# Kernel optimization log

Hardware: AMD Instinct MI355X
Metric: run time of the kernel (lower is better)

Reference implementation:

```python
import jax, jax.numpy as jnp
import numpy as np

B, S, D_IN, D_OUT, DEPTH = 4, 2048, 2048, 2048, 11
N_NODES = 2 ** (DEPTH + 1) - 1  # 4095


def setup_inputs() -> dict:
    key = jax.random.key(0)
    k1, k2, k3 = jax.random.split(key, 3)
    x = jax.random.normal(k1, (B, S, D_IN), dtype=jnp.float32)
    # scale weights like Linear init (~1/sqrt(fan_in)) to keep logits sane
    w_in = jax.random.normal(k2, (N_NODES, D_IN), dtype=jnp.float32) * (1.0 / np.sqrt(D_IN))
    w_out = jax.random.normal(k3, (D_OUT, N_NODES), dtype=jnp.float32) * (1.0 / np.sqrt(N_NODES))
    return {"x": x, "w_in": w_in, "w_out": w_out}


def reference(x, w_in, w_out):
    # x: [B,S,D_in]; w_in: [n_nodes, D_in]; w_out: [D_out, n_nodes]
    b, s, _ = x.shape
    cur = jnp.zeros((b, s), dtype=jnp.int32)
    nodes, logits = [], []
    for _ in range(DEPTH + 1):  # fixed, small depth loop (12 iters)
        nodes.append(cur)
        coeffs = w_in[cur]                       # [B,S,D_in] data-dependent gather
        score = jnp.einsum('bsd,bsd->bs', x, coeffs)  # per-token dot product
        logits.append(score)
        cur = cur * 2 + (score >= 0).astype(jnp.int32) + 1
    all_nodes = jnp.stack(nodes, axis=-1)        # [B,S,depth+1]
    all_logits = jnp.stack(logits, axis=-1)      # [B,S,depth+1]
    sel = w_out.T[all_nodes]                     # [B,S,depth+1,D_out]
    mlp1 = jax.nn.gelu(all_logits, approximate=False)  # torch nn.GELU default = exact erf
    return jnp.einsum('bsl,bslw->bsw', mlp1, sel)      # [B,S,D_out]
```

## Files before the change

### kernel.cpp

```cpp
#include <hip/hip_runtime.h>


#define D_IN    2048
#define D_OUT   2048
#define DEPTHP1 12
#define N_NODES 4095
#define N_TOK   8192
#define N_LEAF  2048

typedef float f4 __attribute__((ext_vector_type(4)));

__global__ __launch_bounds__(256, 4) void fusedA3(
    const float* __restrict__ x,
    const float* __restrict__ w_in,
    const float* __restrict__ w_out,
    float* __restrict__ w_out_t,
    float* __restrict__ s_all,
    int* __restrict__ leaf,
    int* __restrict__ hist) {
    if (blockIdx.x & 1) {
        __shared__ float tile[64][65];
        const int tb = blockIdx.x >> 1;
        const int n0 = (tb & 63) * 64;
        const int j0 = (tb >> 6) * 64;
        const int tx = threadIdx.x & 63;
        const int ty = threadIdx.x >> 6;
        const int n = n0 + tx;
#pragma unroll
        for (int k = 0; k < 16; k++) {
            const int r = ty * 16 + k;
            if (n < N_NODES) tile[r][tx] = w_out[(size_t)(j0 + r) * N_NODES + n];
        }
        __syncthreads();
#pragma unroll
        for (int k = 0; k < 16; k++) {
            const int r = ty * 16 + k;
            const int nn = n0 + r;
            if (nn < N_NODES) w_out_t[(size_t)nn * D_OUT + (j0 + tx)] = tile[tx][r];
        }
        return;
    }

    const int wave  = threadIdx.x >> 6;
    const int lane  = threadIdx.x & 63;
    const int token = (blockIdx.x >> 1) * 4 + wave;

    const float4* xrow = (const float4*)(x + (size_t)token * D_IN);
    float4 xf[8];
#pragma unroll
    for (int c = 0; c < 8; c++) xf[c] = xrow[lane + 64 * c];

    const unsigned voffA = (unsigned)lane * 16u;
    const unsigned voffB = voffA + 4096u;

    int cur = 0;
    float sc[DEPTHP1];
#pragma unroll
    for (int l = 0; l < DEPTHP1; l++) {
        const float* wbase = w_in + (size_t)cur * D_IN;
        f4 w0, w1, w2, w3, w4, w5, w6, w7;
        asm volatile("global_load_dwordx4 %0, %1, %2"             : "=v"(w0) : "v"(voffA), "s"(wbase));
        asm volatile("global_load_dwordx4 %0, %1, %2 offset:1024" : "=v"(w1) : "v"(voffA), "s"(wbase));
        asm volatile("global_load_dwordx4 %0, %1, %2 offset:2048" : "=v"(w2) : "v"(voffA), "s"(wbase));
        asm volatile("global_load_dwordx4 %0, %1, %2 offset:3072" : "=v"(w3) : "v"(voffA), "s"(wbase));
        asm volatile("global_load_dwordx4 %0, %1, %2"             : "=v"(w4) : "v"(voffB), "s"(wbase));
        asm volatile("global_load_dwordx4 %0, %1, %2 offset:1024" : "=v"(w5) : "v"(voffB), "s"(wbase));
        asm volatile("global_load_dwordx4 %0, %1, %2 offset:2048" : "=v"(w6) : "v"(voffB), "s"(wbase));
        asm volatile("global_load_dwordx4 %0, %1, %2 offset:3072" : "=v"(w7) : "v"(voffB), "s"(wbase));
        asm volatile("s_waitcnt vmcnt(0)"
                     : "+v"(w0), "+v"(w1), "+v"(w2), "+v"(w3),
                       "+v"(w4), "+v"(w5), "+v"(w6), "+v"(w7)
                     :: "memory");

        float p0 = 0.f, p1 = 0.f, p2 = 0.f, p3 = 0.f;
        p0 += w0[0]*xf[0].x + w0[1]*xf[0].y + w0[2]*xf[0].z + w0[3]*xf[0].w;
        p0 += w1[0]*xf[1].x + w1[1]*xf[1].y + w1[2]*xf[1].z + w1[3]*xf[1].w;
        p1 += w2[0]*xf[2].x + w2[1]*xf[2].y + w2[2]*xf[2].z + w2[3]*xf[2].w;
        p1 += w3[0]*xf[3].x + w3[1]*xf[3].y + w3[2]*xf[3].z + w3[3]*xf[3].w;
        p2 += w4[0]*xf[4].x + w4[1]*xf[4].y + w4[2]*xf[4].z + w4[3]*xf[4].w;
        p2 += w5[0]*xf[5].x + w5[1]*xf[5].y + w5[2]*xf[5].z + w5[3]*xf[5].w;
        p3 += w6[0]*xf[6].x + w6[1]*xf[6].y + w6[2]*xf[6].z + w6[3]*xf[6].w;
        p3 += w7[0]*xf[7].x + w7[1]*xf[7].y + w7[2]*xf[7].z + w7[3]*xf[7].w;
        float part = (p0 + p1) + (p2 + p3);
#pragma unroll
        for (int off = 32; off >= 1; off >>= 1)
            part += __shfl_xor(part, off, 64);
        const float score = part;
        cur = __builtin_amdgcn_readfirstlane(
                  2 * cur + 1 + (score >= 0.f ? 1 : 0));
        sc[l] = score;
    }
    if (lane == 0) {
        f4* sp = (f4*)(s_all + (size_t)token * DEPTHP1);
        f4 a = {sc[0], sc[1], sc[2],  sc[3]};
        f4 b = {sc[4], sc[5], sc[6],  sc[7]};
        f4 c = {sc[8], sc[9], sc[10], sc[11]};
        sp[0] = a; sp[1] = b; sp[2] = c;
        const int leafid = ((cur - 1) >> 1) - (N_LEAF - 1);
        leaf[token] = leafid;
        atomicAdd(&hist[leafid], 1);
    }
}

__global__ __launch_bounds__(256) void init_counts(int* __restrict__ p) {
    const int i = blockIdx.x * 256 + threadIdx.x;
    if (i < 2 * N_LEAF) p[i] = 0;
}

__global__ __launch_bounds__(256) void scan2048(
    const int* __restrict__ hist, int* __restrict__ offsets ) {
    __shared__ int vals[N_LEAF];
    __shared__ int partial[256];
    const int t = threadIdx.x;
    int sum = 0;
#pragma unroll
    for (int k = 0; k < 8; k++) {
        const int v = hist[t * 8 + k];
        vals[t * 8 + k] = v;
        sum += v;
    }
    partial[t] = sum;
    __syncthreads();
    for (int off = 1; off < 256; off <<= 1) {
        const int v  = partial[t];
        const int vo = (t >= off) ? partial[t - off] : 0;
        __syncthreads();
        partial[t] = v + vo;
        __syncthreads();
    }
    int base = (t > 0) ? partial[t - 1] : 0;
#pragma unroll
    for (int k = 0; k < 8; k++) {
        offsets[t * 8 + k] = base;
        base += vals[t * 8 + k];
    }
    if (t == 255) offsets[N_LEAF] = base;
}

__global__ __launch_bounds__(256) void scatter_tokens3(
    const int* __restrict__ leaf, const int* __restrict__ offsets,
    int* __restrict__ cnt, const float* __restrict__ s_all,
    int* __restrict__ order, float* __restrict__ g_sorted,
    int* __restrict__ lf_sorted) {
    const int t = blockIdx.x * 256 + threadIdx.x;
    if (t < N_TOK) {
        const int lf = leaf[t];
        const int pos = offsets[lf] + atomicAdd(&cnt[lf], 1);
        order[pos] = t;
        lf_sorted[pos] = lf;
#pragma unroll
        for (int l = 0; l < DEPTHP1; l++) {
            const float s = s_all[(size_t)t * DEPTHP1 + l];
            const float g = 0.5f * s * (1.0f + erff(s * 0.70710678118654752f));
            g_sorted[(size_t)pos * DEPTHP1 + l] = g;
        }
    }
}

__global__ __launch_bounds__(256, 2) void phaseB4(
    const float* __restrict__ w_out_t,
    const float* __restrict__ g_sorted,
    const int* __restrict__ lf_sorted,
    const int* __restrict__ order,
    const int* __restrict__ offsets,
    float* __restrict__ out) {
    const int grp = ((blockIdx.x & 7) << 6) | (blockIdx.x >> 3);
    const int lf0 = grp * 4;
    const int start = offsets[lf0];
    const int end   = offsets[lf0 + 4];
    if (start == end) return;
    const int t = threadIdx.x;

    __shared__ float wlds[16 * 1024];
    __shared__ float gslot[2][8][16];
    __shared__ int   ordl[2][8];

    int node[16];
    const int base1 = lf0 + N_LEAF;
#pragma unroll
    for (int l = 0; l <= 9; l++) node[l] = (base1 >> (11 - l)) - 1;
    node[10] = (base1 >> 1) - 1;
    node[11] = (base1 >> 1);
    node[12] = base1 - 1;
    node[13] = base1;
    node[14] = base1 + 1;
    node[15] = base1 + 2;

    for (int half = 0; half < 2; half++) {
        __syncthreads();
#pragma unroll
        for (int k = 0; k < 16; k++)
            ((f4*)wlds)[k * 256 + t] =
                ((const f4*)(w_out_t + (size_t)node[k] * D_OUT + half * 1024))[t];
        __syncthreads();

        int buf = 0;
        for (int cs = start; cs < end; cs += 8, buf ^= 1) {
            if (t < 8) {
                const int pos = cs + t;
#pragma unroll
                for (int s = 0; s < 16; s++) gslot[buf][t][s] = 0.f;
                if (pos < end) {
                    const int lf = lf_sorted[pos];
#pragma unroll
                    for (int l = 0; l <= 9; l++)
                        gslot[buf][t][l] = g_sorted[(size_t)pos * DEPTHP1 + l];
                    gslot[buf][t][10 + ((lf >> 1) & 1)] =
                        g_sorted[(size_t)pos * DEPTHP1 + 10];
                    gslot[buf][t][12 + (lf & 3)] =
                        g_sorted[(size_t)pos * DEPTHP1 + 11];
                    ordl[buf][t] = order[pos];
                }
            }
            __syncthreads();
            const int T = end - cs;
            f4 acc[8];
#pragma unroll
            for (int tt = 0; tt < 8; tt++) acc[tt] = (f4)0.f;
#pragma unroll
            for (int r = 0; r < 16; r++) {
                const f4 w = ((const f4*)wlds)[r * 256 + t];
#pragma unroll
                for (int tt = 0; tt < 8; tt++) {
                    const float g = gslot[buf][tt][r];
                    acc[tt] += g * w;
                }
            }
#pragma unroll
            for (int tt = 0; tt < 8; tt++) {
                if (tt < T) {
                    const int tok = ordl[buf][tt];
                    ((f4*)(out + (size_t)tok * D_OUT + half * 1024))[t] = acc[tt];
                }
            }
        }
    }
}

__global__ __launch_bounds__(256) void transpose_wout64(
    const float* __restrict__ in, float* __restrict__ out) {
    __shared__ float tile[64][65];
    const int n0 = blockIdx.x * 64;
    const int j0 = blockIdx.y * 64;
    const int tx = threadIdx.x;
    const int ty = threadIdx.y;
    const int n = n0 + tx;
#pragma unroll
    for (int k = 0; k < 16; k++) {
        const int r = ty * 16 + k;
        if (n < N_NODES) tile[r][tx] = in[(size_t)(j0 + r) * N_NODES + n];
    }
    __syncthreads();
#pragma unroll
    for (int k = 0; k < 16; k++) {
        const int r = ty * 16 + k;
        const int nn = n0 + r;
        if (nn < N_NODES) out[(size_t)nn * D_OUT + (j0 + tx)] = tile[tx][r];
    }
}

template <bool TRANSPOSED>
__global__ __launch_bounds__(256) void fff_fused(
    const float* __restrict__ x, const float* __restrict__ w_in,
    const float* __restrict__ w_out, float* __restrict__ out) {
    const int wave  = threadIdx.x >> 6;
    const int lane  = threadIdx.x & 63;
    const int token = blockIdx.x * 4 + wave;
    const float4* xrow = (const float4*)(x + (size_t)token * D_IN);
    float xf[32];
#pragma unroll
    for (int c = 0; c < 8; c++) {
        float4 xc = xrow[lane + 64 * c];
        xf[c * 4 + 0] = xc.x; xf[c * 4 + 1] = xc.y;
        xf[c * 4 + 2] = xc.z; xf[c * 4 + 3] = xc.w;
    }
    float acc[32];
#pragma unroll
    for (int k = 0; k < 32; k++) acc[k] = 0.f;
    int cur = 0;
#pragma unroll
    for (int l = 0; l < DEPTHP1; l++) {
        const float4* wrow = (const float4*)(w_in + (size_t)cur * D_IN);
        float part = 0.f;
#pragma unroll
        for (int c = 0; c < 8; c++) {
            float4 wc = wrow[lane + 64 * c];
            part += wc.x * xf[c * 4 + 0]; part += wc.y * xf[c * 4 + 1];
            part += wc.z * xf[c * 4 + 2]; part += wc.w * xf[c * 4 + 3];
        }
#pragma unroll
        for (int off = 32; off >= 1; off >>= 1) part += __shfl_xor(part, off, 64);
        const float score = part;
        const float g = 0.5f * score * (1.0f + erff(score * 0.70710678118654752f));
        if (TRANSPOSED) {
            const float4* orow = (const float4*)(w_out + (size_t)cur * D_OUT);
#pragma unroll
            for (int c = 0; c < 8; c++) {
                float4 oc = orow[lane + 64 * c];
                acc[c * 4 + 0] += g * oc.x; acc[c * 4 + 1] += g * oc.y;
                acc[c * 4 + 2] += g * oc.z; acc[c * 4 + 3] += g * oc.w;
            }
        } else {
#pragma unroll
            for (int c = 0; c < 8; c++)
#pragma unroll
                for (int k = 0; k < 4; k++) {
                    const int j = (lane + 64 * c) * 4 + k;
                    acc[c * 4 + k] += g * w_out[(size_t)j * N_NODES + cur];
                }
        }
        cur = 2 * cur + 1 + (score >= 0.f ? 1 : 0);
    }
    float4* outrow = (float4*)(out + (size_t)token * D_OUT);
#pragma unroll
    for (int c = 0; c < 8; c++) {
        float4 o;
        o.x = acc[c * 4 + 0]; o.y = acc[c * 4 + 1];
        o.z = acc[c * 4 + 2]; o.w = acc[c * 4 + 3];
        outrow[lane + 64 * c] = o;
    }
}

extern "C" void kernel_launch(void* const* d_in, const int* in_sizes, int n_in,
                              void* d_out, int out_size, void* d_ws, size_t ws_size,
                              hipStream_t stream) {
    (void)in_sizes; (void)n_in; (void)out_size;
    const float* x     = (const float*)d_in[0];
    const float* w_in  = (const float*)d_in[1];
    const float* w_out = (const float*)d_in[2];
    float* out = (float*)d_out;

    const size_t wt_bytes   = (size_t)N_NODES * D_OUT * sizeof(float);
    const size_t g_bytes    = (size_t)N_TOK * DEPTHP1 * sizeof(float);
    const size_t leaf_bytes = (size_t)N_TOK * sizeof(int);
    const size_t ord_bytes  = (size_t)N_TOK * sizeof(int);
    const size_t hist_bytes = (size_t)N_LEAF * sizeof(int);
    const size_t cnt_bytes  = (size_t)N_LEAF * sizeof(int);
    const size_t offs_bytes = (size_t)(N_LEAF + 1) * sizeof(int);
    const size_t gs_bytes   = g_bytes;
    const size_t lfs_bytes  = (size_t)N_TOK * sizeof(int);
    const size_t need = wt_bytes + g_bytes + leaf_bytes + ord_bytes +
                        hist_bytes + cnt_bytes + offs_bytes + gs_bytes +
                        lfs_bytes + 64;

    if (ws_size >= need) {
        char* p = (char*)d_ws;
        float* w_out_t  = (float*)p;  p += wt_bytes;
        float* s_all    = (float*)p;  p += g_bytes;
        int*   leaf     = (int*)p;    p += leaf_bytes;
        int*   order    = (int*)p;    p += ord_bytes;
        int*   hist     = (int*)p;    p += hist_bytes;
        int*   cnt      = (int*)p;    p += cnt_bytes;
        int*   offsets  = (int*)p;    p += offs_bytes;
        float* g_sorted = (float*)p;  p += gs_bytes;
        int*   lf_sorted= (int*)p;

        init_counts<<<(2 * N_LEAF + 255) / 256, 256, 0, stream>>>(hist);
        fusedA3<<<4096, 256, 0, stream>>>(x, w_in, w_out, w_out_t,
                                          s_all, leaf, hist);
        scan2048<<<1, 256, 0, stream>>>(hist, offsets);
        scatter_tokens3<<<N_TOK / 256, 256, 0, stream>>>(leaf, offsets, cnt,
                                                         s_all, order, g_sorted,
                                                         lf_sorted);
        phaseB4<<<512, 256, 0, stream>>>(w_out_t, g_sorted, lf_sorted, order,
                                         offsets, out);
    } else if (ws_size >= wt_bytes) {
        float* w_out_t = (float*)d_ws;
        transpose_wout64<<<dim3((N_NODES + 63) / 64, D_OUT / 64), dim3(64, 4),
                           0, stream>>>(w_out, w_out_t);
        fff_fused<true><<<N_TOK / 4, 256, 0, stream>>>(x, w_in, w_out_t, out);
    } else {
        fff_fused<false><<<N_TOK / 4, 256, 0, stream>>>(x, w_in, w_out, out);
    }
}
```

Measured before the change: 261.7 us.

## Hold w_out rows in registers in phase B and precompute padded 16-wide gate vectors

Phase B now keeps the 16 transposed w_out rows for a leaf group in VGPRs instead of LDS, and splits the two output halves across separate blocks (1024 blocks instead of 512). The scatter kernel writes gate values already expanded into a 16-float padded layout, so phase B loads them with vector loads and no per-leaf branching. The transpose moves out of the phase A kernel into its own launch, which also zeroes the histogram and removes the init kernel. The trade is more register pressure per thread in phase B in exchange for no LDS staging of weights and more parallel blocks.

```diff
diff --git a/kernel.cpp b/kernel.cpp
--- a/kernel.cpp
+++ b/kernel.cpp
@@ -10,45 +10,49 @@
 
 typedef float f4 __attribute__((ext_vector_type(4)));
 
-__global__ __launch_bounds__(256, 4) void fusedA3(
+__global__ __launch_bounds__(256) void transpose_wout64z(
+    const float* __restrict__ in, float* __restrict__ out,
+    int* __restrict__ hc ) {
+    __shared__ float tile[64][65];
+    const int fb = blockIdx.y * 64 + blockIdx.x;
+    const int tx = threadIdx.x;
+    const int ty = threadIdx.y;
+    if (fb < 16) {
+        const int i = fb * 256 + ty * 64 + tx;
+        hc[i] = 0;
+    }
+    const int n0 = blockIdx.x * 64;
+    const int j0 = blockIdx.y * 64;
+    const int n = n0 + tx;
+#pragma unroll
+    for (int k = 0; k < 16; k++) {
+        const int r = ty * 16 + k;
+        if (n < N_NODES) tile[r][tx] = in[(size_t)(j0 + r) * N_NODES + n];
+    }
+    __syncthreads();
+#pragma unroll
+    for (int k = 0; k < 16; k++) {
+        const int r = ty * 16 + k;
+        const int nn = n0 + r;
+        if (nn < N_NODES) out[(size_t)nn * D_OUT + (j0 + tx)] = tile[tx][r];
+    }
+}
+
+__global__ __launch_bounds__(256, 4) void phaseA4(
     const float* __restrict__ x,
     const float* __restrict__ w_in,
-    const float* __restrict__ w_out,
-    float* __restrict__ w_out_t,
     float* __restrict__ s_all,
     int* __restrict__ leaf,
     int* __restrict__ hist) {
-    if (blockIdx.x & 1) {
-        __shared__ float tile[64][65];
-        const int tb = blockIdx.x >> 1;
-        const int n0 = (tb & 63) * 64;
-        const int j0 = (tb >> 6) * 64;
-        const int tx = threadIdx.x & 63;
-        const int ty = threadIdx.x >> 6;
-        const int n = n0 + tx;
-#pragma unroll
-        for (int k = 0; k < 16; k++) {
-            const int r = ty * 16 + k;
-            if (n < N_NODES) tile[r][tx] = w_out[(size_t)(j0 + r) * N_NODES + n];
-        }
-        __syncthreads();
-#pragma unroll
-        for (int k = 0; k < 16; k++) {
-            const int r = ty * 16 + k;
-            const int nn = n0 + r;
-            if (nn < N_NODES) w_out_t[(size_t)nn * D_OUT + (j0 + tx)] = tile[tx][r];
-        }
-        return;
-    }
-
     const int wave  = threadIdx.x >> 6;
     const int lane  = threadIdx.x & 63;
-    const int token = (blockIdx.x >> 1) * 4 + wave;
-
-    const float4* xrow = (const float4*)(x + (size_t)token * D_IN);
-    float4 xf[8];
-#pragma unroll
-    for (int c = 0; c < 8; c++) xf[c] = xrow[lane + 64 * c];
+    const int token = blockIdx.x * 4 + wave;
+
+    const f4* xrow = (const f4*)(x + (size_t)token * D_IN);
+    f4 x0 = xrow[lane +   0], x1 = xrow[lane +  64];
+    f4 x2 = xrow[lane + 128], x3 = xrow[lane + 192];
+    f4 x4 = xrow[lane + 256], x5 = xrow[lane + 320];
+    f4 x6 = xrow[lane + 384], x7 = xrow[lane + 448];
 
     const unsigned voffA = (unsigned)lane * 16u;
     const unsigned voffB = voffA + 4096u;
@@ -73,14 +77,17 @@
                      :: "memory");
 
         float p0 = 0.f, p1 = 0.f, p2 = 0.f, p3 = 0.f;
-        p0 += w0[0]*xf[0].x + w0[1]*xf[0].y + w0[2]*xf[0].z + w0[3]*xf[0].w;
-        p0 += w1[0]*xf[1].x + w1[1]*xf[1].y + w1[2]*xf[1].z + w1[3]*xf[1].w;
-        p1 += w2[0]*xf[2].x + w2[1]*xf[2].y + w2[2]*xf[2].z + w2[3]*xf[2].w;
-        p1 += w3[0]*xf[3].x + w3[1]*xf[3].y + w3[2]*xf[3].z + w3[3]*xf[3].w;
-        p2 += w4[0]*xf[4].x + w4[1]*xf[4].y + w4[2]*xf[4].z + w4[3]*xf[4].w;
-        p2 += w5[0]*xf[5].x + w5[1]*xf[5].y + w5[2]*xf[5].z + w5[3]*xf[5].w;
-        p3 += w6[0]*xf[6].x + w6[1]*xf[6].y + w6[2]*xf[6].z + w6[3]*xf[6].w;
-        p3 += w7[0]*xf[7].x + w7[1]*xf[7].y + w7[2]*xf[7].z + w7[3]*xf[7].w;
+        p0 += w0[0]*x0[0] + w0[1]*x0[1] + w0[2]*x0[2] + w0[3]*x0[3];
+        p0 += w1[0]*x1[0] + w1[1]*x1[1] + w1[2]*x1[2] + w1[3]*x1[3];
+        p1 += w2[0]*x2[0] + w2[1]*x2[1] + w2[2]*x2[2] + w2[3]*x2[3];
+        p1 += w3[0]*x3[0] + w3[1]*x3[1] + w3[2]*x3[2] + w3[3]*x3[3];
+        p2 += w4[0]*x4[0] + w4[1]*x4[1] + w4[2]*x4[2] + w4[3]*x4[3];
+        p2 += w5[0]*x5[0] + w5[1]*x5[1] + w5[2]*x5[2] + w5[3]*x5[3];
+        p3 += w6[0]*x6[0] + w6[1]*x6[1] + w6[2]*x6[2] + w6[3]*x6[3];
+        p3 += w7[0]*x7[0] + w7[1]*x7[1] + w7[2]*x7[2] + w7[3]*x7[3];
+        asm volatile("" : "+v"(x0), "+v"(x1), "+v"(x2), "+v"(x3),
+                          "+v"(x4), "+v"(x5), "+v"(x6), "+v"(x7));
+
         float part = (p0 + p1) + (p2 + p3);
 #pragma unroll
         for (int off = 32; off >= 1; off >>= 1)
@@ -102,11 +109,6 @@
     }
 }
 
-__global__ __launch_bounds__(256) void init_counts(int* __restrict__ p) {
-    const int i = blockIdx.x * 256 + threadIdx.x;
-    if (i < 2 * N_LEAF) p[i] = 0;
-}
-
 __global__ __launch_bounds__(256) void scan2048(
     const int* __restrict__ hist, int* __restrict__ offsets ) {
     __shared__ int vals[N_LEAF];
@@ -137,43 +139,47 @@
     if (t == 255) offsets[N_LEAF] = base;
 }
 
-__global__ __launch_bounds__(256) void scatter_tokens3(
+__global__ __launch_bounds__(256) void scatter_tokens4(
     const int* __restrict__ leaf, const int* __restrict__ offsets,
     int* __restrict__ cnt, const float* __restrict__ s_all,
-    int* __restrict__ order, float* __restrict__ g_sorted,
-    int* __restrict__ lf_sorted) {
+    int* __restrict__ order, float* __restrict__ g16 ) {
     const int t = blockIdx.x * 256 + threadIdx.x;
     if (t < N_TOK) {
         const int lf = leaf[t];
         const int pos = offsets[lf] + atomicAdd(&cnt[lf], 1);
         order[pos] = t;
-        lf_sorted[pos] = lf;
+        float g[DEPTHP1];
 #pragma unroll
         for (int l = 0; l < DEPTHP1; l++) {
             const float s = s_all[(size_t)t * DEPTHP1 + l];
-            const float g = 0.5f * s * (1.0f + erff(s * 0.70710678118654752f));
-            g_sorted[(size_t)pos * DEPTHP1 + l] = g;
-        }
-    }
-}
-
-__global__ __launch_bounds__(256, 2) void phaseB4(
+            g[l] = 0.5f * s * (1.0f + erff(s * 0.70710678118654752f));
+        }
+        const int b10 = (lf >> 1) & 1;
+        const int b11 = lf & 3;
+        f4 v0 = {g[0], g[1], g[2], g[3]};
+        f4 v1 = {g[4], g[5], g[6], g[7]};
+        f4 v2 = {g[8], g[9], b10 ? 0.f : g[10], b10 ? g[10] : 0.f};
+        f4 v3 = {b11 == 0 ? g[11] : 0.f, b11 == 1 ? g[11] : 0.f,
+                 b11 == 2 ? g[11] : 0.f, b11 == 3 ? g[11] : 0.f};
+        f4* gp = (f4*)(g16 + (size_t)pos * 16);
+        gp[0] = v0; gp[1] = v1; gp[2] = v2; gp[3] = v3;
+    }
+}
+
+__global__ __launch_bounds__(256, 4) void phaseB5(
     const float* __restrict__ w_out_t,
-    const float* __restrict__ g_sorted,
-    const int* __restrict__ lf_sorted,
+    const float* __restrict__ g16,
     const int* __restrict__ order,
     const int* __restrict__ offsets,
     float* __restrict__ out) {
-    const int grp = ((blockIdx.x & 7) << 6) | (blockIdx.x >> 3);
-    const int lf0 = grp * 4;
+    const int bid  = ((blockIdx.x & 7) << 7) | (blockIdx.x >> 3);
+    const int grp  = bid >> 1;
+    const int half = bid & 1;
+    const int lf0  = grp * 4;
     const int start = offsets[lf0];
     const int end   = offsets[lf0 + 4];
     if (start == end) return;
     const int t = threadIdx.x;
-
-    __shared__ float wlds[16 * 1024];
-    __shared__ float gslot[2][8][16];
-    __shared__ int   ordl[2][8];
 
     int node[16];
     const int base1 = lf0 + N_LEAF;
@@ -186,54 +192,74 @@
     node[14] = base1 + 1;
     node[15] = base1 + 2;
 
-    for (int half = 0; half < 2; half++) {
+    const unsigned voff = (unsigned)t * 16u;
+    const size_t cofs = (size_t)half * 1024;
+    f4 wA0, wA1, wA2, wA3, wA4, wA5, wA6, wA7;
+    f4 wB0, wB1, wB2, wB3, wB4, wB5, wB6, wB7;
+#define LDROW(reg, idx) \
+    asm volatile("global_load_dwordx4 %0, %1, %2" : "=v"(reg) \
+                 : "v"(voff), "s"(w_out_t + (size_t)node[idx] * D_OUT + cofs))
+    LDROW(wA0, 0);  LDROW(wA1, 1);  LDROW(wA2, 2);  LDROW(wA3, 3);
+    LDROW(wA4, 4);  LDROW(wA5, 5);  LDROW(wA6, 6);  LDROW(wA7, 7);
+    LDROW(wB0, 8);  LDROW(wB1, 9);  LDROW(wB2, 10); LDROW(wB3, 11);
+    LDROW(wB4, 12); LDROW(wB5, 13); LDROW(wB6, 14); LDROW(wB7, 15);
+#undef LDROW
+    asm volatile("s_waitcnt vmcnt(0)"
+                 : "+v"(wA0), "+v"(wA1), "+v"(wA2), "+v"(wA3),
+                   "+v"(wA4), "+v"(wA5), "+v"(wA6), "+v"(wA7) :: "memory");
+    asm volatile("" : "+v"(wB0), "+v"(wB1), "+v"(wB2), "+v"(wB3),
+                      "+v"(wB4), "+v"(wB5), "+v"(wB6), "+v"(wB7));
+
+    __shared__ float gsl[128];
+    __shared__ int   ordl[8];
+
+    for (int cs = start; cs < end; cs += 8) {
         __syncthreads();
-#pragma unroll
-        for (int k = 0; k < 16; k++)
-            ((f4*)wlds)[k * 256 + t] =
-                ((const f4*)(w_out_t + (size_t)node[k] * D_OUT + half * 1024))[t];
+        if (t < 32) {
+            const int ti = cs + (t >> 2);
+            ((f4*)gsl)[t] = (ti < end)
+                ? ((const f4*)(g16 + (size_t)cs * 16))[t] : (f4)0.f;
+        } else if (t < 40) {
+            const int ti = cs + (t - 32);
+            ordl[t - 32] = (ti < end) ? order[ti] : 0;
+        }
         __syncthreads();
 
-        int buf = 0;
-        for (int cs = start; cs < end; cs += 8, buf ^= 1) {
-            if (t < 8) {
-                const int pos = cs + t;
-#pragma unroll
-                for (int s = 0; s < 16; s++) gslot[buf][t][s] = 0.f;
-                if (pos < end) {
-                    const int lf = lf_sorted[pos];
-#pragma unroll
-                    for (int l = 0; l <= 9; l++)
-                        gslot[buf][t][l] = g_sorted[(size_t)pos * DEPTHP1 + l];
-                    gslot[buf][t][10 + ((lf >> 1) & 1)] =
-                        g_sorted[(size_t)pos * DEPTHP1 + 10];
-                    gslot[buf][t][12 + (lf & 3)] =
-                        g_sorted[(size_t)pos * DEPTHP1 + 11];
-                    ordl[buf][t] = order[pos];
+        const int T = end - cs;
+        f4 acc[8];
+#pragma unroll
+        for (int tt = 0; tt < 8; tt++) acc[tt] = (f4)0.f;
+
+#pragma unroll
+        for (int rb = 0; rb < 4; rb++) {
+#pragma unroll
+            for (int tt = 0; tt < 8; tt++) {
+                const f4 g4 = ((const f4*)gsl)[tt * 4 + rb];
+                if (rb == 0) {
+                    acc[tt] += g4[0] * wA0; acc[tt] += g4[1] * wA1;
+                    acc[tt] += g4[2] * wA2; acc[tt] += g4[3] * wA3;
+                } else if (rb == 1) {
+                    acc[tt] += g4[0] * wA4; acc[tt] += g4[1] * wA5;
+                    acc[tt] += g4[2] * wA6; acc[tt] += g4[3] * wA7;
+                } else if (rb == 2) {
+                    acc[tt] += g4[0] * wB0; acc[tt] += g4[1] * wB1;
+                    acc[tt] += g4[2] * wB2; acc[tt] += g4[3] * wB3;
+                } else {
+                    acc[tt] += g4[0] * wB4; acc[tt] += g4[1] * wB5;
+                    acc[tt] += g4[2] * wB6; acc[tt] += g4[3] * wB7;
                 }
             }
-            __syncthreads();
-            const int T = end - cs;
-            f4 acc[8];
-#pragma unroll
-            for (int tt = 0; tt < 8; tt++) acc[tt] = (f4)0.f;
-#pragma unroll
-            for (int r = 0; r < 16; r++) {
-                const f4 w = ((const f4*)wlds)[r * 256 + t];
-#pragma unroll
-                for (int tt = 0; tt < 8; tt++) {
-                    const float g = gslot[buf][tt][r];
-                    acc[tt] += g * w;
-                }
+        }
+#pragma unroll
+        for (int tt = 0; tt < 8; tt++) {
+            if (tt < T) {
+                ((f4*)(out + (size_t)ordl[tt] * D_OUT + cofs))[t] = acc[tt];
             }
-#pragma unroll
-            for (int tt = 0; tt < 8; tt++) {
-                if (tt < T) {
-                    const int tok = ordl[buf][tt];
-                    ((f4*)(out + (size_t)tok * D_OUT + half * 1024))[t] = acc[tt];
-                }
-            }
-        }
+        }
+        asm volatile("" : "+v"(wA0), "+v"(wA1), "+v"(wA2), "+v"(wA3),
+                          "+v"(wA4), "+v"(wA5), "+v"(wA6), "+v"(wA7));
+        asm volatile("" : "+v"(wB0), "+v"(wB1), "+v"(wB2), "+v"(wB3),
+                          "+v"(wB4), "+v"(wB5), "+v"(wB6), "+v"(wB7));
     }
 }
 
@@ -331,39 +357,34 @@
     float* out = (float*)d_out;
 
     const size_t wt_bytes   = (size_t)N_NODES * D_OUT * sizeof(float);
-    const size_t g_bytes    = (size_t)N_TOK * DEPTHP1 * sizeof(float);
+    const size_t s_bytes    = (size_t)N_TOK * DEPTHP1 * sizeof(float);
     const size_t leaf_bytes = (size_t)N_TOK * sizeof(int);
     const size_t ord_bytes  = (size_t)N_TOK * sizeof(int);
     const size_t hist_bytes = (size_t)N_LEAF * sizeof(int);
     const size_t cnt_bytes  = (size_t)N_LEAF * sizeof(int);
     const size_t offs_bytes = (size_t)(N_LEAF + 1) * sizeof(int);
-    const size_t gs_bytes   = g_bytes;
-    const size_t lfs_bytes  = (size_t)N_TOK * sizeof(int);
-    const size_t need = wt_bytes + g_bytes + leaf_bytes + ord_bytes +
-                        hist_bytes + cnt_bytes + offs_bytes + gs_bytes +
-                        lfs_bytes + 64;
+    const size_t g16_bytes  = (size_t)N_TOK * 16 * sizeof(float);
+    const size_t need = wt_bytes + s_bytes + leaf_bytes + ord_bytes +
+                        hist_bytes + cnt_bytes + offs_bytes + g16_bytes + 64;
 
     if (ws_size >= need) {
         char* p = (char*)d_ws;
-        float* w_out_t  = (float*)p;  p += wt_bytes;
-        float* s_all    = (float*)p;  p += g_bytes;
-        int*   leaf     = (int*)p;    p += leaf_bytes;
-        int*   order    = (int*)p;    p += ord_bytes;
-        int*   hist     = (int*)p;    p += hist_bytes;
-        int*   cnt      = (int*)p;    p += cnt_bytes;
-        int*   offsets  = (int*)p;    p += offs_bytes;
-        float* g_sorted = (float*)p;  p += gs_bytes;
-        int*   lf_sorted= (int*)p;
-
-        init_counts<<<(2 * N_LEAF + 255) / 256, 256, 0, stream>>>(hist);
-        fusedA3<<<4096, 256, 0, stream>>>(x, w_in, w_out, w_out_t,
-                                          s_all, leaf, hist);
+        float* w_out_t = (float*)p;  p += wt_bytes;
+        float* s_all   = (float*)p;  p += s_bytes;
+        int*   leaf    = (int*)p;    p += leaf_bytes;
+        int*   order   = (int*)p;    p += ord_bytes;
+        int*   hist    = (int*)p;    p += hist_bytes;
+        int*   cnt     = (int*)p;    p += cnt_bytes;
+        int*   offsets = (int*)p;    p += offs_bytes;
+        float* g16     = (float*)p;
+
+        transpose_wout64z<<<dim3(64, 32), dim3(64, 4), 0, stream>>>(
+            w_out, w_out_t, hist);
+        phaseA4<<<N_TOK / 4, 256, 0, stream>>>(x, w_in, s_all, leaf, hist);
         scan2048<<<1, 256, 0, stream>>>(hist, offsets);
-        scatter_tokens3<<<N_TOK / 256, 256, 0, stream>>>(leaf, offsets, cnt,
-                                                         s_all, order, g_sorted,
-                                                         lf_sorted);
-        phaseB4<<<512, 256, 0, stream>>>(w_out_t, g_sorted, lf_sorted, order,
-                                         offsets, out);
+        scatter_tokens4<<<N_TOK / 256, 256, 0, stream>>>(leaf, offsets, cnt,
+                                                         s_all, order, g16);
+        phaseB5<<<1024, 256, 0, stream>>>(w_out_t, g16, order, offsets, out);
     } else if (ws_size >= wt_bytes) {
         float* w_out_t = (float*)d_ws;
         transpose_wout64<<<dim3((N_NODES + 63) / 64, D_OUT / 64), dim3(64, 4),
```

Measured after the change: 286.1 us. 9.3% more time.
